# Optimization experiments

Measured on AMD Instinct MI355X. Metric: run time of the kernel, lower is better.

Reference implementation:

```python
import jax, jax.numpy as jnp
import numpy as np

H_HEADS = 4

def setup_inputs() -> dict:
    key = jax.random.key(0)
    ks = jax.random.split(key, 14)
    B, C, H, W = 8, 512, 32, 32
    r = C // H_HEADS  # SE reduction = h per SelfModule(channel, h)
    s_in = 0.02
    inp = {
        'x': jax.random.normal(ks[0], (B, C, H, W), jnp.float32),
        'wq': jax.random.normal(ks[1], (C, C), jnp.float32) * s_in,
        'bq': jnp.zeros((C,), jnp.float32),
        'wk': jax.random.normal(ks[2], (C, C), jnp.float32) * s_in,
        'bk': jnp.zeros((C,), jnp.float32),
        'wv': jax.random.normal(ks[3], (C, C), jnp.float32) * s_in,
        'bv': jnp.zeros((C,), jnp.float32),
        'fc1_w': jax.random.normal(ks[4], (r, C), jnp.float32) * s_in,
        'fc1_b': jnp.zeros((r,), jnp.float32),
        'fc2_w': jax.random.normal(ks[5], (C, r), jnp.float32) * s_in,
        'fc2_b': jnp.zeros((C,), jnp.float32),
        'gate_w': jax.random.normal(ks[6], (1, C), jnp.float32) * s_in,
        'gate_b': jnp.zeros((1,), jnp.float32),
    }
    return inp

def _conv1x1(y, w, b):
    # y: [B,C,H,W], w: [O,C] (1x1 conv kernel squeezed), b: [O]
    return jnp.einsum('bchw,oc->bohw', y, w) + b[None, :, None, None]

def reference(x, wq, bq, wk, bk, wv, bv, fc1_w, fc1_b, fc2_w, fc2_b, gate_w, gate_b):
    B, C, H, W = x.shape
    h = H_HEADS
    dk = C // h
    N = H * W

    # --- SelfScaling (SE without final sigmoid-in-block; sigmoid applied at mul) ---
    p = x.mean(axis=(2, 3))                                   # [B,C] global avg pool
    f = jax.nn.relu(p @ fc1_w.T + fc1_b) @ fc2_w.T + fc2_b    # [B,C]
    x = x * jax.nn.sigmoid(f)[:, :, None, None] + x

    # --- RTrans: conv1x1 QKV, attention over flattened H*W ---
    q = _conv1x1(x, wq, bq).reshape(B, h, dk, N).transpose(0, 1, 3, 2)  # [B,h,N,dk]
    k = _conv1x1(x, wk, bk).reshape(B, h, dk, N)                        # [B,h,dk,N]
    v = _conv1x1(x, wv, bv).reshape(B, h, dk, N)                        # [B,h,dk,N]
    scale = 1.0 / float(np.sqrt(dk))
    att = jax.nn.softmax(jnp.einsum('bhnd,bhdm->bhnm', q, k) * scale, axis=-1)  # [B,h,N,N]
    o = jnp.einsum('bhdn,bhnm->bhdm', v, att).reshape(B, C, H, W)  # v @ att as in torch

    # --- SelfGating ---
    gate = jax.nn.sigmoid(_conv1x1(o, gate_w, gate_b))  # [B,1,H,W]
    return o * gate + o
```

## Files before the change

kernel.cpp:

```cpp
#include <hip/hip_runtime.h>
#include <hip/hip_bf16.h>

#define B_ 8
#define C_ 512
#define N_ 1024
#define HEADS_ 4
#define DK_ 128
#define R_ 128

typedef float f32x4 __attribute__((ext_vector_type(4)));
typedef __bf16 bf16x8 __attribute__((ext_vector_type(8)));
typedef short short4v __attribute__((ext_vector_type(4)));
typedef unsigned short u16;

constexpr float kScale = 0.08838834764831845f;

#define OFF_P   0u
#define OFF_SS  16384u
#define OFF_WB  32768u
#define OFF_XT  1605632u
#define OFF_QT  9994240u
#define OFF_KT  18382848u
#define OFF_V   26771456u
#define OFF_DEN 35160064u
#define OFF_G   35291136u

__device__ __forceinline__ u16 f2b(float f) {
  __hip_bfloat16 h = __float2bfloat16(f);
  return __builtin_bit_cast(u16, h);
}

typedef const __attribute__((address_space(1))) unsigned int* gptr_t;
typedef __attribute__((address_space(3))) unsigned int* lptr_t;
__device__ __forceinline__ void gload16(const void* g, void* l) {
  __builtin_amdgcn_global_load_lds((gptr_t)g, (lptr_t)l, 16, 0, 0);
}

__device__ __forceinline__ f32x4 mfma16(bf16x8 a, bf16x8 b, f32x4 c) {
  return __builtin_amdgcn_mfma_f32_16x16x32_bf16(a, b, c, 0, 0, 0);
}

#if __has_builtin(__builtin_amdgcn_mfma_f32_16x16x16bf16_1k)
__device__ __forceinline__ f32x4 mfma_k16(short4v a, short4v b, f32x4 c) {
  return __builtin_amdgcn_mfma_f32_16x16x16bf16_1k(a, b, c, 0, 0, 0);
}
#else
__device__ __forceinline__ f32x4 mfma_k16(short4v a, short4v b, f32x4 c) {
  bf16x8 a8 = {}, b8 = {};
  for (int e = 0; e < 4; e++) {
    ((u16*)&a8)[e] = ((u16*)&a)[e];
    ((u16*)&b8)[e] = ((u16*)&b)[e];
  }
  return __builtin_amdgcn_mfma_f32_16x16x32_bf16(a8, b8, c, 0, 0, 0);
}
#endif

__global__ __launch_bounds__(64) void k_pool(const float* __restrict__ x,
                                             float* __restrict__ p) {
  int bc = blockIdx.x, lane = threadIdx.x;
  const float4* row = (const float4*)(x + (size_t)bc * N_);
  float s = 0.f;
  for (int i = lane; i < N_ / 4; i += 64) {
    float4 t = row[i];
    s += t.x + t.y + t.z + t.w;
  }
  for (int o = 32; o > 0; o >>= 1) s += __shfl_down(s, o, 64);
  if (lane == 0) p[bc] = s * (1.0f / N_);
}

__global__ __launch_bounds__(256) void k_se(const float* __restrict__ p,
                                            const float* __restrict__ fc1w,
                                            const float* __restrict__ fc1b,
                                            const float* __restrict__ fc2w,
                                            const float* __restrict__ fc2b,
                                            float* __restrict__ ss) {
  __shared__ float pl[C_];
  __shared__ float f1[R_];
  int b = blockIdx.x, t = threadIdx.x;
  for (int c = t; c < C_; c += 256) pl[c] = p[b * C_ + c];
  __syncthreads();
  if (t < R_) {
    float a = fc1b[t];
    for (int c = 0; c < C_; c++) a += pl[c] * fc1w[t * C_ + c];
    f1[t] = fmaxf(a, 0.f);
  }
  __syncthreads();
  for (int c = t; c < C_; c += 256) {
    float a = fc2b[c];
    for (int j = 0; j < R_; j++) a += f1[j] * fc2w[c * R_ + j];
    ss[b * C_ + c] = 1.f + 1.f / (1.f + __expf(-a));
  }
}

__global__ __launch_bounds__(256) void k_castw_zero(const float* __restrict__ wq,
                                                    const float* __restrict__ wk,
                                                    const float* __restrict__ wv,
                                                    u16* __restrict__ wb,
                                                    float* __restrict__ g) {
  int bid = blockIdx.x;
  if (bid >= 768) {
    g[(bid - 768) * 256 + threadIdx.x] = 0.f;
    return;
  }
  int i = bid * 256 + threadIdx.x;
  int idx = i * 4;
  const float* srcs[3] = {wq, wk, wv};
  int w = idx / (C_ * C_), off = idx % (C_ * C_);
  float4 v = *(const float4*)(srcs[w] + off);
  u16* d = wb + idx;
  d[0] = f2b(v.x); d[1] = f2b(v.y); d[2] = f2b(v.z); d[3] = f2b(v.w);
}

__global__ __launch_bounds__(256) void k_xt(const float* __restrict__ x,
                                            const float* __restrict__ ss,
                                            u16* __restrict__ xt) {
  int b = blockIdx.z, c0 = blockIdx.y * 64, n0 = blockIdx.x * 64;
  __shared__ float tile[64][65];
  int t = threadIdx.x;
  int cr = t >> 4, nc4 = (t & 15) * 4;
  for (int j = 0; j < 4; j++) {
    int c = cr + j * 16;
    float sc = ss[b * C_ + c0 + c];
    float4 v = *(const float4*)(x + ((size_t)b * C_ + c0 + c) * N_ + n0 + nc4);
    tile[c][nc4 + 0] = v.x * sc;
    tile[c][nc4 + 1] = v.y * sc;
    tile[c][nc4 + 2] = v.z * sc;
    tile[c][nc4 + 3] = v.w * sc;
  }
  __syncthreads();
  int nr = t >> 2, cc = (t & 3) * 16;
  u16 ov[16];
  for (int m = 0; m < 16; m++) ov[m] = f2b(tile[cc + m][nr]);
  u16* dst = xt + ((size_t)b * N_ + n0 + nr) * C_ + c0 + cc;
  for (int m = 0; m < 16; m++) dst[m] = ov[m];
}

__global__ __launch_bounds__(256) void k_qkv(const u16* __restrict__ xt,
                                             const u16* __restrict__ wb,
                                             const float* __restrict__ bq,
                                             const float* __restrict__ bk,
                                             const float* __restrict__ bv,
                                             u16* __restrict__ qt,
                                             u16* __restrict__ kt,
                                             u16* __restrict__ v) {
  __shared__ char smem[32768];
  int b = blockIdx.y / 3, sel = blockIdx.y % 3;
  int tile = blockIdx.x;
  const char *Ab, *Bb;
  u16* out;
  const float* bias;
  int mt, nt, rstride;
  size_t xtoff = (size_t)b * N_ * C_;
  if (sel < 2) {
    mt = tile & 7; nt = tile >> 3;
    Ab = (const char*)(xt + xtoff + (size_t)mt * 128 * C_);
    Bb = (const char*)(wb + (size_t)sel * C_ * C_ + (size_t)nt * 128 * C_);
    out = (sel ? kt : qt) + xtoff;
    bias = sel ? bk : bq;
    rstride = C_ * 2;
  } else {
    mt = tile & 3; nt = tile >> 2;
    Ab = (const char*)(wb + (size_t)2 * C_ * C_ + (size_t)mt * 128 * C_);
    Bb = (const char*)(xt + xtoff + (size_t)nt * 128 * C_);
    out = v + (size_t)b * C_ * N_;
    bias = bv;
    rstride = N_ * 2;
  }
  int t = threadIdx.x, lane = t & 63, wid = t >> 6;
  int wr = wid >> 1, wc = wid & 1;
  const f32x4 z4 = {0.f, 0.f, 0.f, 0.f};
  f32x4 acc[4][4];
  for (int i = 0; i < 4; i++)
    for (int j = 0; j < 4; j++) acc[i][j] = z4;

  char* lA = smem;
  char* lB = smem + 16384;
  for (int ko = 0; ko < C_; ko += 64) {
    __syncthreads();
    for (int i = wid; i < 16; i += 4) {
      int beta = i * 1024 + lane * 16;
      int row = beta >> 7, cb = (beta & 127) ^ ((row & 7) << 4);
      gload16(Ab + (size_t)row * 1024 + ko * 2 + cb, lA + beta);
    }
    for (int i = wid; i < 16; i += 4) {
      int beta = i * 1024 + lane * 16;
      int row = beta >> 7, cb = (beta & 127) ^ ((row & 7) << 4);
      gload16(Bb + (size_t)row * 1024 + ko * 2 + cb, lB + beta);
    }
    __syncthreads();
    for (int ks = 0; ks < 2; ks++) {
      int kb = ks * 64 + (lane >> 4) * 16;
      bf16x8 af[4], bfr[4];
      for (int fi = 0; fi < 4; fi++) {
        int row = wr * 64 + fi * 16 + (lane & 15);
        af[fi] = *(const bf16x8*)(lA + row * 128 + (kb ^ ((row & 7) << 4)));
      }
      for (int fj = 0; fj < 4; fj++) {
        int row = wc * 64 + fj * 16 + (lane & 15);
        bfr[fj] = *(const bf16x8*)(lB + row * 128 + (kb ^ ((row & 7) << 4)));
      }
      for (int fi = 0; fi < 4; fi++)
        for (int fj = 0; fj < 4; fj++)
          acc[fi][fj] = mfma16(af[fi], bfr[fj], acc[fi][fj]);
    }
  }
  __syncthreads();
  for (int fi = 0; fi < 4; fi++)
    for (int fj = 0; fj < 4; fj++) {
      int colb = wc * 64 + fj * 16 + (lane & 15);
      for (int r = 0; r < 4; r++) {
        int rowb = wr * 64 + fi * 16 + (lane >> 4) * 4 + r;
        float bva = (sel < 2) ? bias[nt * 128 + colb] : bias[mt * 128 + rowb];
        float val = acc[fi][fj][r] + bva;
        int byte = rowb * 256 + ((colb * 2) ^ ((rowb & 7) << 4));
        *(u16*)(smem + byte) = f2b(val);
      }
    }
  __syncthreads();
  for (int i = t; i < 2048; i += 256) {
    int row = i >> 4, cb = (i & 15) * 16;
    bf16x8 val = *(const bf16x8*)(smem + row * 256 + (cb ^ ((row & 7) << 4)));
    *(bf16x8*)((char*)out + (size_t)(mt * 128 + row) * rstride + nt * 256 + cb) = val;
  }
}

__global__ __launch_bounds__(256) void k_passA(const u16* __restrict__ qt,
                                               const u16* __restrict__ kt,
                                               float* __restrict__ invden) {
  __shared__ char lK[2][32768];
  int bh = blockIdx.x, nb = blockIdx.y * 64;
  int b = bh >> 2, h = bh & 3;
  const char* qb = (const char*)(qt + (size_t)b * N_ * C_ + h * DK_);
  const char* kb = (const char*)(kt + (size_t)b * N_ * C_ + h * DK_);
  int t = threadIdx.x, lane = t & 63, wid = t >> 6;
  bf16x8 aq[4];
  {
    const char* qr = qb + (size_t)(nb + wid * 16 + (lane & 15)) * (C_ * 2);
    for (int ks = 0; ks < 4; ks++)
      aq[ks] = *(const bf16x8*)(qr + ks * 64 + (lane >> 4) * 16);
  }
  float sacc[4] = {0.f, 0.f, 0.f, 0.f};
  const f32x4 z4 = {0.f, 0.f, 0.f, 0.f};
  for (int i = wid; i < 32; i += 4) {
    int beta = i * 1024 + lane * 16;
    int row = beta >> 8, cb = (beta & 255) ^ ((row & 15) << 4);
    gload16(kb + (size_t)row * (C_ * 2) + cb, lK[0] + beta);
  }
  for (int mc = 0; mc < 8; mc++) {
    int cur = mc & 1;
    __syncthreads();
    if (mc < 7) {
      int mnext = (mc + 1) * 128;
      for (int i = wid; i < 32; i += 4) {
        int beta = i * 1024 + lane * 16;
        int row = beta >> 8, cb = (beta & 255) ^ ((row & 15) << 4);
        gload16(kb + (size_t)(mnext + row) * (C_ * 2) + cb, lK[cur ^ 1] + beta);
      }
    }
    for (int fj = 0; fj < 8; fj++) {
      f32x4 s = z4;
      for (int ks = 0; ks < 4; ks++) {
        int row = fj * 16 + (lane & 15);
        bf16x8 bk_ = *(const bf16x8*)(lK[cur] + row * 256 +
                                      ((ks * 64 + (lane >> 4) * 16) ^ ((row & 15) << 4)));
        s = mfma16(aq[ks], bk_, s);
      }
      for (int r = 0; r < 4; r++) sacc[r] += __expf(s[r] * kScale);
    }
  }
  for (int r = 0; r < 4; r++) {
    float vv = sacc[r];
    for (int m = 1; m < 16; m <<= 1) vv += __shfl_xor(vv, m, 64);
    sacc[r] = vv;
  }
  if ((lane & 15) == 0) {
    int n = nb + wid * 16 + (lane >> 4) * 4;
    for (int r = 0; r < 4; r++) invden[(size_t)bh * N_ + n + r] = 1.f / sacc[r];
  }
}

__global__ __launch_bounds__(256) void k_passB(const u16* __restrict__ qt,
                                               const u16* __restrict__ kt,
                                               const u16* __restrict__ v,
                                               const float* __restrict__ invden,
                                               const float* __restrict__ gw,
                                               float* __restrict__ out,
                                               float* __restrict__ g) {
  __shared__ char lQ[2][16384];
  __shared__ char lV[2][16384];
  __shared__ float gacc[64];
  int bh = blockIdx.x, mb = blockIdx.y * 64;
  int b = bh >> 2, h = bh & 3;
  const char* qb = (const char*)(qt + (size_t)b * N_ * C_ + h * DK_);
  const char* kb = (const char*)(kt + (size_t)b * N_ * C_ + h * DK_);
  const char* vb = (const char*)(v + ((size_t)b * C_ + h * DK_) * N_);
  float* ob = out + ((size_t)b * C_ + h * DK_) * N_ + mb;
  const float* idenb = invden + (size_t)bh * N_;
  int t = threadIdx.x, lane = t & 63, wid = t >> 6;
  bf16x8 bkm[4];
  {
    const char* kr = kb + (size_t)(mb + wid * 16 + (lane & 15)) * (C_ * 2);
    for (int ks = 0; ks < 4; ks++)
      bkm[ks] = *(const bf16x8*)(kr + ks * 64 + (lane >> 4) * 16);
  }
  if (t < 64) gacc[t] = 0.f;
  const f32x4 z4 = {0.f, 0.f, 0.f, 0.f};
  f32x4 oacc[8];
  for (int j = 0; j < 8; j++) oacc[j] = z4;

  for (int i = wid; i < 16; i += 4) {
    int beta = i * 1024 + lane * 16;
    int row = beta >> 8, cb = (beta & 255) ^ ((row & 15) << 4);
    gload16(qb + (size_t)row * (C_ * 2) + cb, lQ[0] + beta);
  }
  for (int i = wid; i < 16; i += 4) {
    int beta = i * 1024 + lane * 16;
    int row = beta >> 7, cb = (beta & 127) ^ ((row & 7) << 4);
    gload16(vb + (size_t)row * (N_ * 2) + cb, lV[0] + beta);
  }

  for (int nc = 0; nc < 16; nc++) {
    int n0 = nc * 64, cur = nc & 1;
    __syncthreads();
    if (nc < 15) {
      int nn = n0 + 64;
      for (int i = wid; i < 16; i += 4) {
        int beta = i * 1024 + lane * 16;
        int row = beta >> 8, cb = (beta & 255) ^ ((row & 15) << 4);
        gload16(qb + (size_t)(nn + row) * (C_ * 2) + cb, lQ[cur ^ 1] + beta);
      }
      for (int i = wid; i < 16; i += 4) {
        int beta = i * 1024 + lane * 16;
        int row = beta >> 7, cb = (beta & 127) ^ ((row & 7) << 4);
        gload16(vb + (size_t)row * (N_ * 2) + nn * 2 + cb, lV[cur ^ 1] + beta);
      }
    }
    short4v pf[4];
    for (int fj = 0; fj < 4; fj++) {
      f32x4 s = z4;
      int qrow = fj * 16 + (lane & 15);
      const char* qr = lQ[cur] + qrow * 256;
      int qsw = (qrow & 15) << 4;
      for (int ks = 0; ks < 4; ks++) {
        bf16x8 aq = *(const bf16x8*)(qr + ((ks * 64 + (lane >> 4) * 16) ^ qsw));
        s = mfma16(aq, bkm[ks], s);
      }
      float4 id4 = *(const float4*)(idenb + n0 + fj * 16 + (lane >> 4) * 4);
      short4v pp;
      pp[0] = (short)f2b(__expf(s[0] * kScale) * id4.x);
      pp[1] = (short)f2b(__expf(s[1] * kScale) * id4.y);
      pp[2] = (short)f2b(__expf(s[2] * kScale) * id4.z);
      pp[3] = (short)f2b(__expf(s[3] * kScale) * id4.w);
      pf[fj] = pp;
    }
    for (int fd = 0; fd < 8; fd++) {
      int row = fd * 16 + (lane & 15);
      const char* vr = lV[cur] + row * 128;
      int sw = (row & 7) << 4;
      for (int fj = 0; fj < 4; fj++) {
        short4v av = *(const short4v*)(vr + ((fj * 32 + (lane >> 4) * 8) ^ sw));
        oacc[fd] = mfma_k16(av, pf[fj], oacc[fd]);
      }
    }
  }
  __syncthreads();
  float part = 0.f;
  int mcol = wid * 16 + (lane & 15);
  for (int fd = 0; fd < 8; fd++) {
    float4 gwv = *(const float4*)(gw + h * DK_ + fd * 16 + (lane >> 4) * 4);
    float gwa[4] = {gwv.x, gwv.y, gwv.z, gwv.w};
    for (int r = 0; r < 4; r++) {
      float val = oacc[fd][r];
      int d = fd * 16 + (lane >> 4) * 4 + r;
      ob[(size_t)d * N_ + mcol] = val;
      part += gwa[r] * val;
    }
  }
  atomicAdd(&gacc[mcol], part);
  __syncthreads();
  if (t < 64) atomicAdd(&g[(size_t)b * N_ + mb + t], gacc[t]);
}

__global__ __launch_bounds__(256) void k_gate_apply(const float* __restrict__ g,
                                                    const float* __restrict__ gb,
                                                    float* __restrict__ out) {
  size_t i = ((size_t)blockIdx.x * 256 + threadIdx.x) * 4;
  int b = (int)(i / ((size_t)C_ * N_));
  int n = (int)(i & (N_ - 1));
  float4 gv = *(const float4*)(g + (size_t)b * N_ + n);
  float bias = gb[0];
  float4 v = *(float4*)(out + i);
  v.x *= 1.f + 1.f / (1.f + __expf(-(gv.x + bias)));
  v.y *= 1.f + 1.f / (1.f + __expf(-(gv.y + bias)));
  v.z *= 1.f + 1.f / (1.f + __expf(-(gv.z + bias)));
  v.w *= 1.f + 1.f / (1.f + __expf(-(gv.w + bias)));
  *(float4*)(out + i) = v;
}

extern "C" void kernel_launch(void* const* d_in, const int* in_sizes, int n_in,
                              void* d_out, int out_size, void* d_ws, size_t ws_size,
                              hipStream_t stream) {
  const float* x    = (const float*)d_in[0];
  const float* wq   = (const float*)d_in[1];
  const float* bq   = (const float*)d_in[2];
  const float* wk   = (const float*)d_in[3];
  const float* bk   = (const float*)d_in[4];
  const float* wv   = (const float*)d_in[5];
  const float* bv   = (const float*)d_in[6];
  const float* fc1w = (const float*)d_in[7];
  const float* fc1b = (const float*)d_in[8];
  const float* fc2w = (const float*)d_in[9];
  const float* fc2b = (const float*)d_in[10];
  const float* gw   = (const float*)d_in[11];
  const float* gb   = (const float*)d_in[12];
  float* out = (float*)d_out;
  char* ws = (char*)d_ws;

  float* p   = (float*)(ws + OFF_P);
  float* ssc = (float*)(ws + OFF_SS);
  u16* wb  = (u16*)(ws + OFF_WB);
  u16* xt  = (u16*)(ws + OFF_XT);
  u16* qt  = (u16*)(ws + OFF_QT);
  u16* kt  = (u16*)(ws + OFF_KT);
  u16* v   = (u16*)(ws + OFF_V);
  float* den = (float*)(ws + OFF_DEN);
  float* g   = (float*)(ws + OFF_G);

  k_pool<<<B_ * C_, 64, 0, stream>>>(x, p);
  k_castw_zero<<<800, 256, 0, stream>>>(wq, wk, wv, wb, g);
  k_se<<<B_, 256, 0, stream>>>(p, fc1w, fc1b, fc2w, fc2b, ssc);
  k_xt<<<dim3(16, 8, B_), 256, 0, stream>>>(x, ssc, xt);
  k_qkv<<<dim3(32, B_ * 3), 256, 0, stream>>>(xt, wb, bq, bk, bv, qt, kt, v);
  k_passA<<<dim3(32, 16), 256, 0, stream>>>(qt, kt, den);
  k_passB<<<dim3(32, 16), 256, 0, stream>>>(qt, kt, v, den, gw, out, g);
  k_gate_apply<<<B_ * C_ * N_ / 1024, 256, 0, stream>>>(g, gb, out);
}
```

Measured before the change: 120.5 us.

## Materialize exp scores once and turn attention output into a plain GEMM

Pass A now writes the unnormalized bf16 exp(QK^T) matrix to workspace alongside the row denominators. V is pre-scaled by the reciprocal denominators, and pass B becomes a tiled V·E^T GEMM split in two along the reduction dimension, with the halves summed in the gate kernel. This removes the second QK^T computation and its exponentials. In exchange it adds a large round trip of the score matrix through HBM and an extra fp32 partial output buffer.

```diff
diff --git a/kernel.cpp b/kernel.cpp
--- a/kernel.cpp
+++ b/kernel.cpp
@@ -24,10 +24,15 @@
 #define OFF_V   26771456u
 #define OFF_DEN 35160064u
 #define OFF_G   35291136u
+#define OFF_O1  35323904u
+#define OFF_E   52101120u
 
 __device__ __forceinline__ u16 f2b(float f) {
   __hip_bfloat16 h = __float2bfloat16(f);
   return __builtin_bit_cast(u16, h);
+}
+__device__ __forceinline__ float b2f(u16 u) {
+  return __builtin_bit_cast(float, (unsigned)u << 16);
 }
 
 typedef const __attribute__((address_space(1))) unsigned int* gptr_t;
@@ -39,21 +44,6 @@
 __device__ __forceinline__ f32x4 mfma16(bf16x8 a, bf16x8 b, f32x4 c) {
   return __builtin_amdgcn_mfma_f32_16x16x32_bf16(a, b, c, 0, 0, 0);
 }
-
-#if __has_builtin(__builtin_amdgcn_mfma_f32_16x16x16bf16_1k)
-__device__ __forceinline__ f32x4 mfma_k16(short4v a, short4v b, f32x4 c) {
-  return __builtin_amdgcn_mfma_f32_16x16x16bf16_1k(a, b, c, 0, 0, 0);
-}
-#else
-__device__ __forceinline__ f32x4 mfma_k16(short4v a, short4v b, f32x4 c) {
-  bf16x8 a8 = {}, b8 = {};
-  for (int e = 0; e < 4; e++) {
-    ((u16*)&a8)[e] = ((u16*)&a)[e];
-    ((u16*)&b8)[e] = ((u16*)&b)[e];
-  }
-  return __builtin_amdgcn_mfma_f32_16x16x32_bf16(a8, b8, c, 0, 0, 0);
-}
-#endif
 
 __global__ __launch_bounds__(64) void k_pool(const float* __restrict__ x,
                                              float* __restrict__ p) {
@@ -226,26 +216,30 @@
 
 __global__ __launch_bounds__(256) void k_passA(const u16* __restrict__ qt,
                                                const u16* __restrict__ kt,
+                                               u16* __restrict__ et,
                                                float* __restrict__ invden) {
   __shared__ char lK[2][32768];
+  __shared__ char lE[16384];
   int bh = blockIdx.x, nb = blockIdx.y * 64;
   int b = bh >> 2, h = bh & 3;
   const char* qb = (const char*)(qt + (size_t)b * N_ * C_ + h * DK_);
   const char* kb = (const char*)(kt + (size_t)b * N_ * C_ + h * DK_);
+  char* etb = (char*)(et + (size_t)bh * N_ * N_);
   int t = threadIdx.x, lane = t & 63, wid = t >> 6;
-  bf16x8 aq[4];
+  bf16x8 bq[4];
   {
     const char* qr = qb + (size_t)(nb + wid * 16 + (lane & 15)) * (C_ * 2);
     for (int ks = 0; ks < 4; ks++)
-      aq[ks] = *(const bf16x8*)(qr + ks * 64 + (lane >> 4) * 16);
-  }
-  float sacc[4] = {0.f, 0.f, 0.f, 0.f};
+      bq[ks] = *(const bf16x8*)(qr + ks * 64 + (lane >> 4) * 16);
+  }
+  float dpart = 0.f;
   const f32x4 z4 = {0.f, 0.f, 0.f, 0.f};
   for (int i = wid; i < 32; i += 4) {
     int beta = i * 1024 + lane * 16;
     int row = beta >> 8, cb = (beta & 255) ^ ((row & 15) << 4);
     gload16(kb + (size_t)row * (C_ * 2) + cb, lK[0] + beta);
   }
+  int nloc2 = (wid * 16 + (lane & 15)) * 2;
   for (int mc = 0; mc < 8; mc++) {
     int cur = mc & 1;
     __syncthreads();
@@ -261,140 +255,145 @@
       f32x4 s = z4;
       for (int ks = 0; ks < 4; ks++) {
         int row = fj * 16 + (lane & 15);
-        bf16x8 bk_ = *(const bf16x8*)(lK[cur] + row * 256 +
-                                      ((ks * 64 + (lane >> 4) * 16) ^ ((row & 15) << 4)));
-        s = mfma16(aq[ks], bk_, s);
-      }
-      for (int r = 0; r < 4; r++) sacc[r] += __expf(s[r] * kScale);
-    }
-  }
-  for (int r = 0; r < 4; r++) {
-    float vv = sacc[r];
-    for (int m = 1; m < 16; m <<= 1) vv += __shfl_xor(vv, m, 64);
-    sacc[r] = vv;
-  }
-  if ((lane & 15) == 0) {
-    int n = nb + wid * 16 + (lane >> 4) * 4;
-    for (int r = 0; r < 4; r++) invden[(size_t)bh * N_ + n + r] = 1.f / sacc[r];
-  }
-}
-
-__global__ __launch_bounds__(256) void k_passB(const u16* __restrict__ qt,
-                                               const u16* __restrict__ kt,
-                                               const u16* __restrict__ v,
-                                               const float* __restrict__ invden,
+        bf16x8 ak = *(const bf16x8*)(lK[cur] + row * 256 +
+                                     ((ks * 64 + (lane >> 4) * 16) ^ ((row & 15) << 4)));
+        s = mfma16(ak, bq[ks], s);
+      }
+      for (int r = 0; r < 4; r++) {
+        float e = __expf(s[r] * kScale);
+        dpart += e;
+        int m = fj * 16 + (lane >> 4) * 4 + r;
+        *(u16*)(lE + m * 128 + (nloc2 ^ ((m & 7) << 4))) = f2b(e);
+      }
+    }
+    __syncthreads();
+    for (int i = t; i < 1024; i += 256) {
+      int row = i >> 3, c16 = (i & 7) * 16;
+      bf16x8 val = *(const bf16x8*)(lE + row * 128 + (c16 ^ ((row & 7) << 4)));
+      *(bf16x8*)(etb + (size_t)(mc * 128 + row) * (N_ * 2) + nb * 2 + c16) = val;
+    }
+  }
+  dpart += __shfl_xor(dpart, 16, 64);
+  dpart += __shfl_xor(dpart, 32, 64);
+  if (lane < 16)
+    invden[(size_t)bh * N_ + nb + wid * 16 + lane] = 1.f / dpart;
+}
+
+__global__ __launch_bounds__(256) void k_vscale(u16* __restrict__ v,
+                                                const float* __restrict__ invden) {
+  size_t i = ((size_t)blockIdx.x * 256 + threadIdx.x) * 8;
+  int n = (int)(i & (N_ - 1));
+  int bc = (int)(i >> 10);
+  int b = bc >> 9, c = bc & 511, h = c >> 7;
+  const float* iv = invden + ((size_t)(b * 4 + h)) * N_ + n;
+  float4 iv0 = *(const float4*)(iv);
+  float4 iv1 = *(const float4*)(iv + 4);
+  u16* p = v + i;
+  short4v a = *(short4v*)p, bb = *(short4v*)(p + 4);
+  u16 o[8];
+  o[0] = f2b(b2f((u16)a[0]) * iv0.x);
+  o[1] = f2b(b2f((u16)a[1]) * iv0.y);
+  o[2] = f2b(b2f((u16)a[2]) * iv0.z);
+  o[3] = f2b(b2f((u16)a[3]) * iv0.w);
+  o[4] = f2b(b2f((u16)bb[0]) * iv1.x);
+  o[5] = f2b(b2f((u16)bb[1]) * iv1.y);
+  o[6] = f2b(b2f((u16)bb[2]) * iv1.z);
+  o[7] = f2b(b2f((u16)bb[3]) * iv1.w);
+  short4v r0 = {(short)o[0], (short)o[1], (short)o[2], (short)o[3]};
+  short4v r1 = {(short)o[4], (short)o[5], (short)o[6], (short)o[7]};
+  *(short4v*)p = r0;
+  *(short4v*)(p + 4) = r1;
+}
+
+__global__ __launch_bounds__(256) void k_passB(const u16* __restrict__ v,
+                                               const u16* __restrict__ et,
                                                const float* __restrict__ gw,
-                                               float* __restrict__ out,
+                                               float* __restrict__ out0,
+                                               float* __restrict__ o1,
                                                float* __restrict__ g) {
-  __shared__ char lQ[2][16384];
-  __shared__ char lV[2][16384];
-  __shared__ float gacc[64];
-  int bh = blockIdx.x, mb = blockIdx.y * 64;
+  __shared__ char smem[32768];
+  __shared__ float gacc[128];
+  int bh = blockIdx.x, mt = blockIdx.y, nh = blockIdx.z;
   int b = bh >> 2, h = bh & 3;
-  const char* qb = (const char*)(qt + (size_t)b * N_ * C_ + h * DK_);
-  const char* kb = (const char*)(kt + (size_t)b * N_ * C_ + h * DK_);
-  const char* vb = (const char*)(v + ((size_t)b * C_ + h * DK_) * N_);
-  float* ob = out + ((size_t)b * C_ + h * DK_) * N_ + mb;
-  const float* idenb = invden + (size_t)bh * N_;
+  const char* Ab = (const char*)(v + ((size_t)b * C_ + h * DK_) * N_) + nh * 1024;
+  const char* Bb = (const char*)(et + (size_t)bh * N_ * N_ + (size_t)mt * 128 * N_) + nh * 1024;
+  float* ob = (nh ? o1 : out0) + ((size_t)b * C_ + h * DK_) * N_ + mt * 128;
   int t = threadIdx.x, lane = t & 63, wid = t >> 6;
-  bf16x8 bkm[4];
-  {
-    const char* kr = kb + (size_t)(mb + wid * 16 + (lane & 15)) * (C_ * 2);
-    for (int ks = 0; ks < 4; ks++)
-      bkm[ks] = *(const bf16x8*)(kr + ks * 64 + (lane >> 4) * 16);
-  }
-  if (t < 64) gacc[t] = 0.f;
+  int wr = wid >> 1, wc = wid & 1;
+  if (t < 128) gacc[t] = 0.f;
   const f32x4 z4 = {0.f, 0.f, 0.f, 0.f};
-  f32x4 oacc[8];
-  for (int j = 0; j < 8; j++) oacc[j] = z4;
-
-  for (int i = wid; i < 16; i += 4) {
-    int beta = i * 1024 + lane * 16;
-    int row = beta >> 8, cb = (beta & 255) ^ ((row & 15) << 4);
-    gload16(qb + (size_t)row * (C_ * 2) + cb, lQ[0] + beta);
-  }
-  for (int i = wid; i < 16; i += 4) {
-    int beta = i * 1024 + lane * 16;
-    int row = beta >> 7, cb = (beta & 127) ^ ((row & 7) << 4);
-    gload16(vb + (size_t)row * (N_ * 2) + cb, lV[0] + beta);
-  }
-
-  for (int nc = 0; nc < 16; nc++) {
-    int n0 = nc * 64, cur = nc & 1;
-    __syncthreads();
-    if (nc < 15) {
-      int nn = n0 + 64;
-      for (int i = wid; i < 16; i += 4) {
-        int beta = i * 1024 + lane * 16;
-        int row = beta >> 8, cb = (beta & 255) ^ ((row & 15) << 4);
-        gload16(qb + (size_t)(nn + row) * (C_ * 2) + cb, lQ[cur ^ 1] + beta);
-      }
-      for (int i = wid; i < 16; i += 4) {
-        int beta = i * 1024 + lane * 16;
-        int row = beta >> 7, cb = (beta & 127) ^ ((row & 7) << 4);
-        gload16(vb + (size_t)row * (N_ * 2) + nn * 2 + cb, lV[cur ^ 1] + beta);
-      }
-    }
-    short4v pf[4];
-    for (int fj = 0; fj < 4; fj++) {
-      f32x4 s = z4;
-      int qrow = fj * 16 + (lane & 15);
-      const char* qr = lQ[cur] + qrow * 256;
-      int qsw = (qrow & 15) << 4;
-      for (int ks = 0; ks < 4; ks++) {
-        bf16x8 aq = *(const bf16x8*)(qr + ((ks * 64 + (lane >> 4) * 16) ^ qsw));
-        s = mfma16(aq, bkm[ks], s);
-      }
-      float4 id4 = *(const float4*)(idenb + n0 + fj * 16 + (lane >> 4) * 4);
-      short4v pp;
-      pp[0] = (short)f2b(__expf(s[0] * kScale) * id4.x);
-      pp[1] = (short)f2b(__expf(s[1] * kScale) * id4.y);
-      pp[2] = (short)f2b(__expf(s[2] * kScale) * id4.z);
-      pp[3] = (short)f2b(__expf(s[3] * kScale) * id4.w);
-      pf[fj] = pp;
-    }
-    for (int fd = 0; fd < 8; fd++) {
-      int row = fd * 16 + (lane & 15);
-      const char* vr = lV[cur] + row * 128;
-      int sw = (row & 7) << 4;
+  f32x4 acc[4][4];
+  for (int i = 0; i < 4; i++)
+    for (int j = 0; j < 4; j++) acc[i][j] = z4;
+
+  char* lA = smem;
+  char* lB = smem + 16384;
+  for (int ko = 0; ko < 512; ko += 64) {
+    __syncthreads();
+    for (int i = wid; i < 16; i += 4) {
+      int beta = i * 1024 + lane * 16;
+      int row = beta >> 7, cb = (beta & 127) ^ ((row & 7) << 4);
+      gload16(Ab + (size_t)row * 2048 + ko * 2 + cb, lA + beta);
+    }
+    for (int i = wid; i < 16; i += 4) {
+      int beta = i * 1024 + lane * 16;
+      int row = beta >> 7, cb = (beta & 127) ^ ((row & 7) << 4);
+      gload16(Bb + (size_t)row * 2048 + ko * 2 + cb, lB + beta);
+    }
+    __syncthreads();
+    for (int ks = 0; ks < 2; ks++) {
+      int kb = ks * 64 + (lane >> 4) * 16;
+      bf16x8 af[4], bfr[4];
+      for (int fi = 0; fi < 4; fi++) {
+        int row = wr * 64 + fi * 16 + (lane & 15);
+        af[fi] = *(const bf16x8*)(lA + row * 128 + (kb ^ ((row & 7) << 4)));
+      }
       for (int fj = 0; fj < 4; fj++) {
-        short4v av = *(const short4v*)(vr + ((fj * 32 + (lane >> 4) * 8) ^ sw));
-        oacc[fd] = mfma_k16(av, pf[fj], oacc[fd]);
-      }
-    }
-  }
-  __syncthreads();
-  float part = 0.f;
-  int mcol = wid * 16 + (lane & 15);
-  for (int fd = 0; fd < 8; fd++) {
-    float4 gwv = *(const float4*)(gw + h * DK_ + fd * 16 + (lane >> 4) * 4);
-    float gwa[4] = {gwv.x, gwv.y, gwv.z, gwv.w};
-    for (int r = 0; r < 4; r++) {
-      float val = oacc[fd][r];
-      int d = fd * 16 + (lane >> 4) * 4 + r;
-      ob[(size_t)d * N_ + mcol] = val;
-      part += gwa[r] * val;
-    }
-  }
-  atomicAdd(&gacc[mcol], part);
-  __syncthreads();
-  if (t < 64) atomicAdd(&g[(size_t)b * N_ + mb + t], gacc[t]);
+        int row = wc * 64 + fj * 16 + (lane & 15);
+        bfr[fj] = *(const bf16x8*)(lB + row * 128 + (kb ^ ((row & 7) << 4)));
+      }
+      for (int fi = 0; fi < 4; fi++)
+        for (int fj = 0; fj < 4; fj++)
+          acc[fi][fj] = mfma16(af[fi], bfr[fj], acc[fi][fj]);
+    }
+  }
+  for (int fj = 0; fj < 4; fj++) {
+    int mcol = wc * 64 + fj * 16 + (lane & 15);
+    float part = 0.f;
+    for (int fi = 0; fi < 4; fi++) {
+      int d = wr * 64 + fi * 16 + (lane >> 4) * 4;
+      float4 gwv = *(const float4*)(gw + h * DK_ + d);
+      float ga[4] = {gwv.x, gwv.y, gwv.z, gwv.w};
+      for (int r = 0; r < 4; r++) {
+        float val = acc[fi][fj][r];
+        ob[(size_t)(d + r) * N_ + mcol] = val;
+        part += ga[r] * val;
+      }
+    }
+    atomicAdd(&gacc[mcol], part);
+  }
+  __syncthreads();
+  if (t < 128) atomicAdd(&g[(size_t)b * N_ + mt * 128 + t], gacc[t]);
 }
 
 __global__ __launch_bounds__(256) void k_gate_apply(const float* __restrict__ g,
                                                     const float* __restrict__ gb,
+                                                    const float* __restrict__ o1,
                                                     float* __restrict__ out) {
   size_t i = ((size_t)blockIdx.x * 256 + threadIdx.x) * 4;
   int b = (int)(i / ((size_t)C_ * N_));
   int n = (int)(i & (N_ - 1));
   float4 gv = *(const float4*)(g + (size_t)b * N_ + n);
   float bias = gb[0];
-  float4 v = *(float4*)(out + i);
-  v.x *= 1.f + 1.f / (1.f + __expf(-(gv.x + bias)));
-  v.y *= 1.f + 1.f / (1.f + __expf(-(gv.y + bias)));
-  v.z *= 1.f + 1.f / (1.f + __expf(-(gv.z + bias)));
-  v.w *= 1.f + 1.f / (1.f + __expf(-(gv.w + bias)));
-  *(float4*)(out + i) = v;
+  float4 v0 = *(float4*)(out + i);
+  float4 v1 = *(const float4*)(o1 + i);
+  float ox = v0.x + v1.x, oy = v0.y + v1.y, oz = v0.z + v1.z, ow = v0.w + v1.w;
+  ox *= 1.f + 1.f / (1.f + __expf(-(gv.x + bias)));
+  oy *= 1.f + 1.f / (1.f + __expf(-(gv.y + bias)));
+  oz *= 1.f + 1.f / (1.f + __expf(-(gv.z + bias)));
+  ow *= 1.f + 1.f / (1.f + __expf(-(gv.w + bias)));
+  float4 r = {ox, oy, oz, ow};
+  *(float4*)(out + i) = r;
 }
 
 extern "C" void kernel_launch(void* const* d_in, const int* in_sizes, int n_in,
@@ -425,13 +424,16 @@
   u16* v   = (u16*)(ws + OFF_V);
   float* den = (float*)(ws + OFF_DEN);
   float* g   = (float*)(ws + OFF_G);
+  float* o1  = (float*)(ws + OFF_O1);
+  u16* et  = (u16*)(ws + OFF_E);
 
   k_pool<<<B_ * C_, 64, 0, stream>>>(x, p);
   k_castw_zero<<<800, 256, 0, stream>>>(wq, wk, wv, wb, g);
   k_se<<<B_, 256, 0, stream>>>(p, fc1w, fc1b, fc2w, fc2b, ssc);
   k_xt<<<dim3(16, 8, B_), 256, 0, stream>>>(x, ssc, xt);
   k_qkv<<<dim3(32, B_ * 3), 256, 0, stream>>>(xt, wb, bq, bk, bv, qt, kt, v);
-  k_passA<<<dim3(32, 16), 256, 0, stream>>>(qt, kt, den);
-  k_passB<<<dim3(32, 16), 256, 0, stream>>>(qt, kt, v, den, gw, out, g);
-  k_gate_apply<<<B_ * C_ * N_ / 1024, 256, 0, stream>>>(g, gb, out);
-}
+  k_passA<<<dim3(32, 16), 256, 0, stream>>>(qt, kt, et, den);
+  k_vscale<<<2048, 256, 0, stream>>>(v, den);
+  k_passB<<<dim3(32, 8, 2), 256, 0, stream>>>(v, et, gw, out, o1, g);
+  k_gate_apply<<<B_ * C_ * N_ / 1024, 256, 0, stream>>>(g, gb, o1, out);
+}
```

Result: no change. 120.3 us (-0.2%).
